# Kernel optimization log

Hardware: AMD Instinct MI355X
Metric: run time of the kernel (lower is better)

The kernel has to match this reference:

```python
import jax, jax.numpy as jnp
import numpy as np

H, NH, L, S, B, V = 512, 8, 6, 2048, 2, 32000
DH = H // NH
EPS = 1e-5


def posenc(h, s):
    pos = jnp.arange(s, dtype=jnp.float32)[:, None]
    div = jnp.power(10000.0, jnp.arange(0, h, 2, dtype=jnp.float32) / h)
    pe = jnp.zeros((s, h), dtype=jnp.float32)
    pe = pe.at[:, 0::2].set(jnp.sin(pos / div))
    pe = pe.at[:, 1::2].set(jnp.cos(pos / div))
    return pe


def layernorm(x, g, b):
    mu = jnp.mean(x, axis=-1, keepdims=True)
    var = jnp.mean(jnp.square(x - mu), axis=-1, keepdims=True)
    return (x - mu) * jax.lax.rsqrt(var + EPS) * g + b


def setup_inputs() -> dict:
    key = jax.random.key(0)
    ks = jax.random.split(key, 16)
    sc = 0.02
    return {
        "src": jax.random.randint(ks[0], (B, S), 0, V),
        "mask": jnp.ones((B, 1, 1, S), dtype=jnp.int32),
        "emb": jax.random.normal(ks[1], (V, H), jnp.float32) * sc,
        "Wq": jax.random.normal(ks[2], (L, H, H), jnp.float32) * sc,
        "bq": jnp.zeros((L, H), jnp.float32),
        "Wk": jax.random.normal(ks[3], (L, H, H), jnp.float32) * sc,
        "bk": jnp.zeros((L, H), jnp.float32),
        "Wv": jax.random.normal(ks[4], (L, H, H), jnp.float32) * sc,
        "bv": jnp.zeros((L, H), jnp.float32),
        "Wo": jax.random.normal(ks[5], (L, H, H), jnp.float32) * sc,
        "bo": jnp.zeros((L, H), jnp.float32),
        "gamma": jnp.ones((L, H), jnp.float32),
        "beta": jnp.zeros((L, H), jnp.float32),
        "W1": jax.random.normal(ks[6], (L, H, 4 * H), jnp.float32) * sc,
        "b1": jnp.zeros((L, 4 * H), jnp.float32),
        "W2": jax.random.normal(ks[7], (L, 4 * H, H), jnp.float32) * sc,
        "b2": jnp.zeros((L, H), jnp.float32),
    }


def reference(src, mask, emb, Wq, bq, Wk, bk, Wv, bv, Wo, bo, gamma, beta, W1, b1, W2, b2):
    x = emb[src] + posenc(H, S)[None, :, :]  # [B,S,H]
    for i in range(L):
        q = (x @ Wq[i] + bq[i]).reshape(B, S, NH, DH).transpose(0, 2, 1, 3)
        k = (x @ Wk[i] + bk[i]).reshape(B, S, NH, DH).transpose(0, 2, 1, 3)
        v = (x @ Wv[i] + bv[i]).reshape(B, S, NH, DH).transpose(0, 2, 1, 3)
        scores = jnp.einsum("bhqd,bhkd->bhqk", q, k) / jnp.sqrt(jnp.float32(DH))
        scores = jnp.where(mask == 0, jnp.float32(-1e20), scores)
        attn = jax.nn.softmax(scores, axis=-1)
        av = jnp.einsum("bhqk,bhkd->bhqd", attn, v)
        attn_out = av.transpose(0, 2, 1, 3).reshape(B, S, H) @ Wo[i] + bo[i]
        # NOTE: same LayerNorm params applied to both sublayers (as in source)
        res = x + layernorm(attn_out, gamma[i], beta[i])
        ffn = jax.nn.relu(res @ W1[i] + b1[i]) @ W2[i] + b2[i]
        x = res + layernorm(ffn, gamma[i], beta[i])
    return x
```

## Files before the change

### kernel.cpp

```cpp
#include <hip/hip_runtime.h>
#include <math.h>

#define HDIM 512
#define NHEAD 8
#define NLAYER 6
#define SEQ 2048
#define BATCH 2
#define DHEAD 64
#define TOKENS (BATCH*SEQ)
#define FFND (4*HDIM)
#define QSTR 1536

typedef unsigned short u16;
typedef __attribute__((ext_vector_type(8))) short short8;
typedef __attribute__((ext_vector_type(4))) float f32x4;

__device__ __forceinline__ u16 f2b(float f) {
  unsigned u = __float_as_uint(f);
  u += 0x7FFFu + ((u >> 16) & 1u);
  return (u16)(u >> 16);
}

__device__ __forceinline__ void gload_lds16(const u16* g, u16* l) {
  __builtin_amdgcn_global_load_lds((const __attribute__((address_space(1))) void*)g,
                                   (__attribute__((address_space(3))) void*)l, 16, 0, 0);
}

__global__ void embed_pe(const int* __restrict__ src, const float* __restrict__ emb,
                         float* __restrict__ X, u16* __restrict__ Xb) {
  int tok = blockIdx.x;
  int lane = threadIdx.x;
  int s = tok & (SEQ - 1);
  int c0 = lane * 8;
  const float* e = emb + (long)src[tok] * HDIM + c0;
  float v[8];
#pragma unroll
  for (int j = 0; j < 8; j++) {
    int c = c0 + j;
    float arg = (float)s * exp2f(-(float)(c & ~1) * 0.02595256917f);
    v[j] = e[j] + ((c & 1) ? cosf(arg) : sinf(arg));
  }
  float* xp = X + (long)tok * HDIM + c0;
#pragma unroll
  for (int j = 0; j < 8; j++) xp[j] = v[j];
  u16 hb[8];
#pragma unroll
  for (int j = 0; j < 8; j++) hb[j] = f2b(v[j]);
  uint4 pk;
  pk.x = hb[0] | ((unsigned)hb[1] << 16);
  pk.y = hb[2] | ((unsigned)hb[3] << 16);
  pk.z = hb[4] | ((unsigned)hb[5] << 16);
  pk.w = hb[6] | ((unsigned)hb[7] << 16);
  *(uint4*)(Xb + (long)tok * HDIM + c0) = pk;
}

__global__ __launch_bounds__(256) void prep_weights(
    const float* __restrict__ Wq, const float* __restrict__ Wk, const float* __restrict__ Wv,
    const float* __restrict__ Wo, const float* __restrict__ W1, const float* __restrict__ W2,
    const float* __restrict__ bq, const float* __restrict__ bk, const float* __restrict__ bv,
    u16* __restrict__ Wqkvt, u16* __restrict__ Wot, u16* __restrict__ W1t, u16* __restrict__ W2t,
    float* __restrict__ bqkv) {
  int t = blockIdx.x;
  int tid = threadIdx.x;
  if (t == 768) {
    for (int i = tid; i < 1536; i += 256)
      bqkv[i] = (i < 512) ? bq[i] : (i < 1024) ? bk[i - 512] : bv[i - 1024];
    return;
  }
  const float* src; u16* dst; int K, N, kt, nt; long drow0 = 0;
  if (t < 192)      { int m = t / 64, r = t % 64; src = (m==0)?Wq:(m==1)?Wk:Wv; dst = Wqkvt; drow0 = (long)m*512; K=512;  N=512;  kt=r/8;  nt=r%8; }
  else if (t < 256) { int r = t - 192; src = Wo; dst = Wot; K=512;  N=512;  kt=r/8;  nt=r%8; }
  else if (t < 512) { int r = t - 256; src = W1; dst = W1t; K=512;  N=2048; kt=r/32; nt=r%32; }
  else              { int r = t - 512; src = W2; dst = W2t; K=2048; N=512;  kt=r/8;  nt=r%8; }
  __shared__ __align__(16) u16 Lt[64 * 72];
  int kl = tid >> 2;
#pragma unroll
  for (int rr = 0; rr < 4; rr++) {
    int cl = (tid & 3) * 4 + rr * 16;
    float4 v = *(const float4*)(src + (long)(kt * 64 + kl) * N + nt * 64 + cl);
    Lt[(cl + 0) * 72 + kl] = f2b(v.x);
    Lt[(cl + 1) * 72 + kl] = f2b(v.y);
    Lt[(cl + 2) * 72 + kl] = f2b(v.z);
    Lt[(cl + 3) * 72 + kl] = f2b(v.w);
  }
  __syncthreads();
  int nl = tid >> 2;
  int kc = (tid & 3) * 16;
  u16* dp = dst + (drow0 + nt * 64 + nl) * (long)K + kt * 64 + kc;
  *(uint4*)dp       = *(const uint4*)&Lt[nl * 72 + kc];
  *(uint4*)(dp + 8) = *(const uint4*)&Lt[nl * 72 + kc + 8];
}

__global__ __launch_bounds__(256) void vtranspose(const u16* __restrict__ QKV,
                                                  u16* __restrict__ Vtb) {
  __shared__ __align__(16) u16 Lt[64 * 72];
  int tid = threadIdx.x;
  int bh = blockIdx.y, b = bh >> 3, h = bh & 7;
  int s0 = blockIdx.x * 64;
  const u16* vsrc = QKV + (long)(b * SEQ + s0) * QSTR + 1024 + h * DHEAD;
  int key = tid >> 2, dc = (tid & 3) * 16;
  const u16* vp = vsrc + (long)key * QSTR + dc;
  uint4 v0 = *(const uint4*)vp;
  uint4 v1 = *(const uint4*)(vp + 8);
  unsigned vr[8] = { v0.x, v0.y, v0.z, v0.w, v1.x, v1.y, v1.z, v1.w };
#pragma unroll
  for (int j = 0; j < 8; j++) {
    Lt[(dc + 2 * j) * 72 + key]     = (u16)vr[j];
    Lt[(dc + 2 * j + 1) * 72 + key] = (u16)(vr[j] >> 16);
  }
  __syncthreads();
  int d = tid >> 2, kc = (tid & 3) * 16;
  u16* dst = Vtb + ((long)bh * DHEAD + d) * SEQ + s0 + kc;
  *(uint4*)dst       = *(const uint4*)&Lt[d * 72 + kc];
  *(uint4*)(dst + 8) = *(const uint4*)&Lt[d * 72 + kc + 8];
}

template <int BN, int KSPLIT, bool RELU, bool WF32, bool WB16>
__global__ __launch_bounds__(256) void gemm_tn(const u16* __restrict__ A,
                                               const u16* __restrict__ Bt,
                                               const float* __restrict__ bias,
                                               float* __restrict__ Cf,
                                               u16* __restrict__ Cb,
                                               int M, int N, int K) {
  constexpr int NF = BN / 32;
  __shared__ __align__(16) u16 As[2][128 * 32];
  __shared__ __align__(16) u16 Bs[2][BN * 32];
  int tid = threadIdx.x;
  int wave = tid >> 6, lane = tid & 63;
  int ln = lane & 15, hi = lane >> 4;
  int wm = wave >> 1, wn = wave & 1;
  int m0 = blockIdx.y * 128, n0 = blockIdx.x * BN;
  int z = (KSPLIT > 1) ? blockIdx.z : 0;
  int Ks = K / KSPLIT;
  const u16* Ab = A + z * Ks;
  const u16* Bb = Bt + z * Ks;

  f32x4 acc[4][NF] = {};

  int srow = lane >> 2;
  int skc  = (lane & 3) * 8;

  auto issue = [&](int kt, int buf) {
    int k0 = kt * 32;
#pragma unroll
    for (int j = 0; j < 2; j++) {
      int row = (wave * 2 + j) * 16 + srow;
      gload_lds16(Ab + (long)(m0 + row) * K + k0 + skc, &As[buf][row * 32 + skc]);
    }
#pragma unroll
    for (int j = 0; j < BN / 64; j++) {
      int row = (wave * (BN / 64) + j) * 16 + srow;
      gload_lds16(Bb + (long)(n0 + row) * K + k0 + skc, &Bs[buf][row * 32 + skc]);
    }
  };

  int NT = Ks / 32;
  issue(0, 0);
  __syncthreads();
  for (int kt = 0; kt < NT; kt++) {
    int buf = kt & 1;
    if (kt + 1 < NT) issue(kt + 1, buf ^ 1);
    short8 af[4], bf[NF];
#pragma unroll
    for (int mt = 0; mt < 4; mt++)
      af[mt] = *(const short8*)&As[buf][(wm * 64 + mt * 16 + ln) * 32 + 8 * hi];
#pragma unroll
    for (int nt = 0; nt < NF; nt++)
      bf[nt] = *(const short8*)&Bs[buf][(wn * (BN / 2) + nt * 16 + ln) * 32 + 8 * hi];
#pragma unroll
    for (int mt = 0; mt < 4; mt++)
#pragma unroll
      for (int nt = 0; nt < NF; nt++)
        acc[mt][nt] = __builtin_amdgcn_mfma_f32_16x16x32_bf16(af[mt], bf[nt], acc[mt][nt], 0, 0, 0);
    __syncthreads();
  }

  float* Cz = WF32 ? (Cf + (long)z * M * N) : nullptr;
#pragma unroll
  for (int mt = 0; mt < 4; mt++)
#pragma unroll
    for (int nt = 0; nt < NF; nt++)
#pragma unroll
      for (int r = 0; r < 4; r++) {
        int row = m0 + wm * 64 + mt * 16 + hi * 4 + r;
        int col = n0 + wn * (BN / 2) + nt * 16 + ln;
        float v = acc[mt][nt][r];
        if (KSPLIT == 1 || z == 0) v += bias[col];
        if (RELU) v = fmaxf(v, 0.0f);
        if (WF32) Cz[(long)row * N + col] = v;
        if (WB16) Cb[(long)row * N + col] = f2b(v);
      }
}

__global__ __launch_bounds__(256) void attention(const u16* __restrict__ QKV,
                                                 const u16* __restrict__ Vtb,
                                                 const int* __restrict__ mask,
                                                 u16* __restrict__ Og) {
  __shared__ __align__(16) u16 Ks[2][2][64 * 32];
  __shared__ __align__(16) u16 Vs[2][2][64 * 32];
  __shared__ __align__(16) u16 P[4 * 16 * 72];
  int tid = threadIdx.x, w = tid >> 6, lane = tid & 63;
  int ln = lane & 15, hi = lane >> 4;
  int bh = blockIdx.y, b = bh >> 3, h = bh & 7;
  int q0 = blockIdx.x * 64 + w * 16;
  const u16* qbase = QKV + (long)b * SEQ * QSTR + h * DHEAD;
  const u16* kbase = qbase + 512;
  const u16* vtbase = Vtb + (long)bh * DHEAD * SEQ;
  const int* mrow = mask + b * SEQ;
  u16* Pw = P + w * 16 * 72;

  short8 qf[2];
#pragma unroll
  for (int ks = 0; ks < 2; ks++)
    qf[ks] = *(const short8*)(qbase + (long)(q0 + ln) * QSTR + ks * 32 + 8 * hi);

  f32x4 o[4] = {};
  float lst[4] = {0.0f, 0.0f, 0.0f, 0.0f};

  int srow = w * 16 + (lane >> 2);
  int sc = (lane & 3) * 8;

  auto issue = [&](int t, int buf) {
    long kk = (long)t * 64;
    const u16* kg = kbase + (kk + srow) * QSTR + sc;
    gload_lds16(kg,      &Ks[buf][0][srow * 32 + sc]);
    gload_lds16(kg + 32, &Ks[buf][1][srow * 32 + sc]);
    const u16* vg = vtbase + (long)srow * SEQ + kk + sc;
    gload_lds16(vg,      &Vs[buf][0][srow * 32 + sc]);
    gload_lds16(vg + 32, &Vs[buf][1][srow * 32 + sc]);
  };

  const int NT = SEQ / 64;
  issue(0, 0);
  __syncthreads();
  for (int t = 0; t < NT; t++) {
    int buf = t & 1;
    if (t + 1 < NT) issue(t + 1, buf ^ 1);
    int k0 = t * 64;

    f32x4 s[4] = {};
#pragma unroll
    for (int ks = 0; ks < 2; ks++)
#pragma unroll
      for (int nt = 0; nt < 4; nt++) {
        short8 bf = *(const short8*)&Ks[buf][ks][(nt * 16 + ln) * 32 + 8 * hi];
        s[nt] = __builtin_amdgcn_mfma_f32_16x16x32_bf16(qf[ks], bf, s[nt], 0, 0, 0);
      }
    int mv[4];
#pragma unroll
    for (int nt = 0; nt < 4; nt++) mv[nt] = mrow[k0 + nt * 16 + ln];
#pragma unroll
    for (int r = 0; r < 4; r++) {
#pragma unroll
      for (int nt = 0; nt < 4; nt++) {
        float p = (mv[nt] == 0) ? 0.0f : __expf(s[nt][r] * 0.125f);
        lst[r] += p;
        Pw[(hi * 4 + r) * 72 + ((nt * 16 + ln) ^ (8 * hi))] = f2b(p);
      }
    }
    short8 pa[2];
#pragma unroll
    for (int ka = 0; ka < 2; ka++)
      pa[ka] = *(const short8*)&Pw[ln * 72 + (ka * 32 + ((8 * hi) ^ (8 * (ln >> 2))))];
#pragma unroll
    for (int nt = 0; nt < 4; nt++) {
      short8 bv0 = *(const short8*)&Vs[buf][0][(nt * 16 + ln) * 32 + 8 * hi];
      short8 bv1 = *(const short8*)&Vs[buf][1][(nt * 16 + ln) * 32 + 8 * hi];
      o[nt] = __builtin_amdgcn_mfma_f32_16x16x32_bf16(pa[0], bv0, o[nt], 0, 0, 0);
      o[nt] = __builtin_amdgcn_mfma_f32_16x16x32_bf16(pa[1], bv1, o[nt], 0, 0, 0);
    }
    __syncthreads();
  }

#pragma unroll
  for (int r = 0; r < 4; r++) {
    float l = lst[r];
    l += __shfl_xor(l, 1);
    l += __shfl_xor(l, 2);
    l += __shfl_xor(l, 4);
    l += __shfl_xor(l, 8);
    lst[r] = 1.0f / l;
  }

  u16* obase = Og + (long)b * SEQ * HDIM + h * DHEAD;
#pragma unroll
  for (int r = 0; r < 4; r++) {
    int srow2 = q0 + hi * 4 + r;
#pragma unroll
    for (int nt = 0; nt < 4; nt++)
      obase[(long)srow2 * HDIM + nt * 16 + ln] = f2b(o[nt][r] * lst[r]);
  }
}

__global__ __launch_bounds__(256) void ln_residual(const float* __restrict__ Xin,
                                                   const float* __restrict__ T0,
                                                   const float* __restrict__ T1,
                                                   const float* __restrict__ gamma,
                                                   const float* __restrict__ beta,
                                                   float* __restrict__ Xout,
                                                   u16* __restrict__ Xb) {
  int tid = threadIdx.x, w = tid >> 6, lane = tid & 63;
  int row = blockIdx.x * 4 + w;
  const float* t0 = T0 + (long)row * HDIM;
  const float* t1 = T1 + (long)row * HDIM;
  int c0 = lane * 8;
  float v[8];
  {
    float4 a0 = *(const float4*)(t0 + c0);
    float4 b0 = *(const float4*)(t0 + c0 + 4);
    float4 a1 = *(const float4*)(t1 + c0);
    float4 b1 = *(const float4*)(t1 + c0 + 4);
    v[0] = a0.x + a1.x; v[1] = a0.y + a1.y; v[2] = a0.z + a1.z; v[3] = a0.w + a1.w;
    v[4] = b0.x + b1.x; v[5] = b0.y + b1.y; v[6] = b0.z + b1.z; v[7] = b0.w + b1.w;
  }
  float sum = 0.0f;
#pragma unroll
  for (int j = 0; j < 8; j++) sum += v[j];
#pragma unroll
  for (int off = 32; off; off >>= 1) sum += __shfl_xor(sum, off);
  float mu = sum * (1.0f / HDIM);
  float sq = 0.0f;
#pragma unroll
  for (int j = 0; j < 8; j++) { float d = v[j] - mu; sq += d * d; }
#pragma unroll
  for (int off = 32; off; off >>= 1) sq += __shfl_xor(sq, off);
  float rs = rsqrtf(sq * (1.0f / HDIM) + 1e-5f);
  const float* xin = Xin + (long)row * HDIM + c0;
  float* xout = Xout + (long)row * HDIM + c0;
  u16 hb[8];
#pragma unroll
  for (int j = 0; j < 8; j++) {
    int c = c0 + j;
    float y = xin[j] + (v[j] - mu) * rs * gamma[c] + beta[c];
    xout[j] = y;
    hb[j] = f2b(y);
  }
  uint4 pk;
  pk.x = hb[0] | ((unsigned)hb[1] << 16);
  pk.y = hb[2] | ((unsigned)hb[3] << 16);
  pk.z = hb[4] | ((unsigned)hb[5] << 16);
  pk.w = hb[6] | ((unsigned)hb[7] << 16);
  *(uint4*)(Xb + (long)row * HDIM + c0) = pk;
}

extern "C" void kernel_launch(void* const* d_in, const int* in_sizes, int n_in,
                              void* d_out, int out_size, void* d_ws, size_t ws_size,
                              hipStream_t stream) {
  const int*   src   = (const int*)d_in[0];
  const int*   mask  = (const int*)d_in[1];
  const float* emb   = (const float*)d_in[2];
  const float* Wq    = (const float*)d_in[3];
  const float* bq    = (const float*)d_in[4];
  const float* Wk    = (const float*)d_in[5];
  const float* bk    = (const float*)d_in[6];
  const float* Wv    = (const float*)d_in[7];
  const float* bv    = (const float*)d_in[8];
  const float* Wo    = (const float*)d_in[9];
  const float* bo    = (const float*)d_in[10];
  const float* gamma = (const float*)d_in[11];
  const float* beta  = (const float*)d_in[12];
  const float* W1    = (const float*)d_in[13];
  const float* b1    = (const float*)d_in[14];
  const float* W2    = (const float*)d_in[15];
  const float* b2    = (const float*)d_in[16];

  char* ws = (char*)d_ws;
  float* X     = (float*)(ws);
  u16*   Xb    = (u16*)(ws + (8ll << 20));
  u16*   QKVb  = (u16*)(ws + (12ll << 20));
  u16*   Mb    = (u16*)(ws + (12ll << 20));
  u16*   AVb   = (u16*)(ws + (24ll << 20));
  float* T     = (float*)(ws + (28ll << 20));
  u16*   Wqkvt = (u16*)(ws + (44ll << 20));
  u16*   Wot   = (u16*)(ws + (45ll << 20) + (512ll << 10));
  u16*   W1t   = (u16*)(ws + (46ll << 20));
  u16*   W2t   = (u16*)(ws + (48ll << 20));
  float* bqkv  = (float*)(ws + (50ll << 20));
  u16*   Vtb   = (u16*)(ws + (51ll << 20));
  float* T1    = T + (long)TOKENS * HDIM;

  embed_pe<<<dim3(TOKENS), dim3(64), 0, stream>>>(src, emb, X, Xb);

  for (int i = 0; i < NLAYER; i++) {
    long wo = (long)i * HDIM * HDIM;
    prep_weights<<<dim3(769), 256, 0, stream>>>(
        Wq + wo, Wk + wo, Wv + wo, Wo + wo,
        W1 + (long)i * HDIM * FFND, W2 + (long)i * FFND * HDIM,
        bq + i * HDIM, bk + i * HDIM, bv + i * HDIM,
        Wqkvt, Wot, W1t, W2t, bqkv);

    gemm_tn<128, 1, false, false, true><<<dim3(QSTR / 128, TOKENS / 128), 256, 0, stream>>>(
        Xb, Wqkvt, bqkv, nullptr, QKVb, TOKENS, QSTR, HDIM);

    vtranspose<<<dim3(SEQ / 64, BATCH * NHEAD), 256, 0, stream>>>(QKVb, Vtb);

    attention<<<dim3(SEQ / 64, BATCH * NHEAD), 256, 0, stream>>>(QKVb, Vtb, mask, AVb);

    gemm_tn<64, 2, false, true, false><<<dim3(HDIM / 64, TOKENS / 128, 2), 256, 0, stream>>>(
        AVb, Wot, bo + i * HDIM, T, nullptr, TOKENS, HDIM, HDIM);

    ln_residual<<<dim3(TOKENS / 4), 256, 0, stream>>>(X, T, T1, gamma + i * HDIM,
                                                      beta + i * HDIM, X, Xb);

    gemm_tn<128, 1, true, false, true><<<dim3(FFND / 128, TOKENS / 128), 256, 0, stream>>>(
        Xb, W1t, b1 + (long)i * FFND, nullptr, Mb, TOKENS, FFND, HDIM);

    gemm_tn<64, 2, false, true, false><<<dim3(HDIM / 64, TOKENS / 128, 2), 256, 0, stream>>>(
        Mb, W2t, b2 + i * HDIM, T, nullptr, TOKENS, HDIM, FFND);

    ln_residual<<<dim3(TOKENS / 4), 256, 0, stream>>>(X, T, T1, gamma + i * HDIM,
                                                      beta + i * HDIM, X, Xb);
  }

  hipMemcpyAsync(d_out, X, (size_t)TOKENS * HDIM * sizeof(float),
                 hipMemcpyDeviceToDevice, stream);
}
```

Before: 1.064 ms.

## Compute transposed S^T tiles in attention to keep P in registers, skipping LDS

The attention kernel now computes K·Q^T, so the score tile comes out transposed and each lane's probabilities can be packed straight into the B operand of the PV MFMA. A cross-lane shuffle replaces the round trip through shared memory for P. K/V tiles move to an XOR-swizzled 64-wide LDS layout with permuted key rows. Mask loads are vectorised and row sums are reduced once at the end. The output is staged through LDS for coalesced 16-byte stores, and bf16 packing uses the hardware v_cvt_pk_bf16_f32 instruction. The intent is to cut LDS traffic, bank conflicts and store inefficiency, at the cost of tricky lane/key index mapping that must be exactly right.

New measurement: 1.070 ms. About the same (+0.6%).

```diff
diff --git a/kernel.cpp b/kernel.cpp
--- a/kernel.cpp
+++ b/kernel.cpp
@@ -19,6 +19,12 @@
   unsigned u = __float_as_uint(f);
   u += 0x7FFFu + ((u >> 16) & 1u);
   return (u16)(u >> 16);
+}
+
+__device__ __forceinline__ unsigned cvtpk_bf16(float lo, float hi) {
+  unsigned r;
+  asm("v_cvt_pk_bf16_f32 %0, %1, %2" : "=v"(r) : "v"(lo), "v"(hi));
+  return r;
 }
 
 __device__ __forceinline__ void gload_lds16(const u16* g, u16* l) {
@@ -196,99 +202,130 @@
                                                  const u16* __restrict__ Vtb,
                                                  const int* __restrict__ mask,
                                                  u16* __restrict__ Og) {
-  __shared__ __align__(16) u16 Ks[2][2][64 * 32];
-  __shared__ __align__(16) u16 Vs[2][2][64 * 32];
-  __shared__ __align__(16) u16 P[4 * 16 * 72];
+  __shared__ __align__(16) u16 Ks[2][64 * 64];
+  __shared__ __align__(16) u16 Vs[2][64 * 64];
   int tid = threadIdx.x, w = tid >> 6, lane = tid & 63;
   int ln = lane & 15, hi = lane >> 4;
+  int h0 = hi & 1, h1 = hi >> 1, ln7 = ln & 7;
   int bh = blockIdx.y, b = bh >> 3, h = bh & 7;
   int q0 = blockIdx.x * 64 + w * 16;
   const u16* qbase = QKV + (long)b * SEQ * QSTR + h * DHEAD;
   const u16* kbase = qbase + 512;
   const u16* vtbase = Vtb + (long)bh * DHEAD * SEQ;
   const int* mrow = mask + b * SEQ;
-  u16* Pw = P + w * 16 * 72;
 
   short8 qf[2];
 #pragma unroll
   for (int ks = 0; ks < 2; ks++)
     qf[ks] = *(const short8*)(qbase + (long)(q0 + ln) * QSTR + ks * 32 + 8 * hi);
 
+  int sr0 = tid >> 3, sc = tid & 7;
+  const u16 *kp0, *kp1, *vp0, *vp1;
+  {
+    int r1 = sr0 + 32;
+    int key0 = (sr0 & 7) | ((sr0 & 0x18) << 1) | ((sr0 & 0x20) >> 2);
+    int key1 = (r1 & 7) | ((r1 & 0x18) << 1) | ((r1 & 0x20) >> 2);
+    kp0 = kbase + (long)key0 * QSTR + (sc ^ (sr0 & 7)) * 8;
+    kp1 = kbase + (long)key1 * QSTR + (sc ^ (r1 & 7)) * 8;
+    vp0 = vtbase + (long)sr0 * SEQ + (sc ^ (sr0 & 7)) * 8;
+    vp1 = vtbase + (long)r1 * SEQ + (sc ^ (r1 & 7)) * 8;
+  }
+  int d0 = sr0 * 64 + sc * 8, d1 = d0 + 2048;
+
+  auto issue = [&](int t, int buf) {
+    long ko = (long)t * (64 * QSTR);
+    int vo = t * 64;
+    gload_lds16(kp0 + ko, &Ks[buf][d0]);
+    gload_lds16(kp1 + ko, &Ks[buf][d1]);
+    gload_lds16(vp0 + vo, &Vs[buf][d0]);
+    gload_lds16(vp1 + vo, &Vs[buf][d1]);
+  };
+
   f32x4 o[4] = {};
-  float lst[4] = {0.0f, 0.0f, 0.0f, 0.0f};
-
-  int srow = w * 16 + (lane >> 2);
-  int sc = (lane & 3) * 8;
-
-  auto issue = [&](int t, int buf) {
-    long kk = (long)t * 64;
-    const u16* kg = kbase + (kk + srow) * QSTR + sc;
-    gload_lds16(kg,      &Ks[buf][0][srow * 32 + sc]);
-    gload_lds16(kg + 32, &Ks[buf][1][srow * 32 + sc]);
-    const u16* vg = vtbase + (long)srow * SEQ + kk + sc;
-    gload_lds16(vg,      &Vs[buf][0][srow * 32 + sc]);
-    gload_lds16(vg + 32, &Vs[buf][1][srow * 32 + sc]);
-  };
-
+  float lsum = 0.0f;
   const int NT = SEQ / 64;
   issue(0, 0);
   __syncthreads();
   for (int t = 0; t < NT; t++) {
     int buf = t & 1;
+    const int* mbase = mrow + t * 64 + 16 * h1 + 4 * h0;
+    int4 mv[4];
+    mv[0] = *(const int4*)(mbase);
+    mv[1] = *(const int4*)(mbase + 32);
+    mv[2] = *(const int4*)(mbase + 8);
+    mv[3] = *(const int4*)(mbase + 40);
     if (t + 1 < NT) issue(t + 1, buf ^ 1);
-    int k0 = t * 64;
 
     f32x4 s[4] = {};
 #pragma unroll
     for (int ks = 0; ks < 2; ks++)
 #pragma unroll
-      for (int nt = 0; nt < 4; nt++) {
-        short8 bf = *(const short8*)&Ks[buf][ks][(nt * 16 + ln) * 32 + 8 * hi];
-        s[nt] = __builtin_amdgcn_mfma_f32_16x16x32_bf16(qf[ks], bf, s[nt], 0, 0, 0);
+      for (int kb = 0; kb < 4; kb++) {
+        short8 kf = *(const short8*)&Ks[buf][(kb * 16 + ln) * 64 + (((ks << 2) + hi) ^ ln7) * 8];
+        s[kb] = __builtin_amdgcn_mfma_f32_16x16x32_bf16(kf, qf[ks], s[kb], 0, 0, 0);
       }
-    int mv[4];
-#pragma unroll
-    for (int nt = 0; nt < 4; nt++) mv[nt] = mrow[k0 + nt * 16 + ln];
-#pragma unroll
-    for (int r = 0; r < 4; r++) {
-#pragma unroll
-      for (int nt = 0; nt < 4; nt++) {
-        float p = (mv[nt] == 0) ? 0.0f : __expf(s[nt][r] * 0.125f);
-        lst[r] += p;
-        Pw[(hi * 4 + r) * 72 + ((nt * 16 + ln) ^ (8 * hi))] = f2b(p);
+
+    unsigned D[4][2];
+#pragma unroll
+    for (int kb = 0; kb < 4; kb++) {
+      float p[4];
+#pragma unroll
+      for (int r = 0; r < 4; r++) {
+        float pv = __expf(s[kb][r] * 0.125f);
+        int m = (&mv[kb].x)[r];
+        pv = m ? pv : 0.0f;
+        lsum += pv;
+        p[r] = pv;
       }
+      D[kb][0] = cvtpk_bf16(p[0], p[1]);
+      D[kb][1] = cvtpk_bf16(p[2], p[3]);
     }
-    short8 pa[2];
-#pragma unroll
-    for (int ka = 0; ka < 2; ka++)
-      pa[ka] = *(const short8*)&Pw[ln * 72 + (ka * 32 + ((8 * hi) ^ (8 * (ln >> 2))))];
-#pragma unroll
-    for (int nt = 0; nt < 4; nt++) {
-      short8 bv0 = *(const short8*)&Vs[buf][0][(nt * 16 + ln) * 32 + 8 * hi];
-      short8 bv1 = *(const short8*)&Vs[buf][1][(nt * 16 + ln) * 32 + 8 * hi];
-      o[nt] = __builtin_amdgcn_mfma_f32_16x16x32_bf16(pa[0], bv0, o[nt], 0, 0, 0);
-      o[nt] = __builtin_amdgcn_mfma_f32_16x16x32_bf16(pa[1], bv1, o[nt], 0, 0, 0);
+
+    short8 pb[2];
+#pragma unroll
+    for (int ks = 0; ks < 2; ks++) {
+      unsigned own0 = h0 ? D[2 + ks][0] : D[ks][0];
+      unsigned own1 = h0 ? D[2 + ks][1] : D[ks][1];
+      unsigned snd0 = h0 ? D[ks][0] : D[2 + ks][0];
+      unsigned snd1 = h0 ? D[ks][1] : D[2 + ks][1];
+      unsigned rc0 = (unsigned)__shfl_xor((int)snd0, 16);
+      unsigned rc1 = (unsigned)__shfl_xor((int)snd1, 16);
+      union { unsigned u[4]; short8 v; } pu;
+      pu.u[0] = h0 ? rc0 : own0;
+      pu.u[1] = h0 ? rc1 : own1;
+      pu.u[2] = h0 ? own0 : rc0;
+      pu.u[3] = h0 ? own1 : rc1;
+      pb[ks] = pu.v;
     }
+
+#pragma unroll
+    for (int ks = 0; ks < 2; ks++)
+#pragma unroll
+      for (int mb = 0; mb < 4; mb++) {
+        short8 vf = *(const short8*)&Vs[buf][(mb * 16 + ln) * 64 + (((ks << 2) + hi) ^ ln7) * 8];
+        o[mb] = __builtin_amdgcn_mfma_f32_16x16x32_bf16(vf, pb[ks], o[mb], 0, 0, 0);
+      }
     __syncthreads();
   }
 
-#pragma unroll
-  for (int r = 0; r < 4; r++) {
-    float l = lst[r];
-    l += __shfl_xor(l, 1);
-    l += __shfl_xor(l, 2);
-    l += __shfl_xor(l, 4);
-    l += __shfl_xor(l, 8);
-    lst[r] = 1.0f / l;
-  }
-
+  lsum += __shfl_xor(lsum, 16);
+  lsum += __shfl_xor(lsum, 32);
+  float rl = 1.0f / lsum;
+
+  u16* Ot = &Ks[0][0] + w * 1024;
+#pragma unroll
+  for (int mb = 0; mb < 4; mb++) {
+    *(unsigned*)&Ot[ln * 64 + mb * 16 + hi * 4 + 0] = cvtpk_bf16(o[mb][0] * rl, o[mb][1] * rl);
+    *(unsigned*)&Ot[ln * 64 + mb * 16 + hi * 4 + 2] = cvtpk_bf16(o[mb][2] * rl, o[mb][3] * rl);
+  }
+  __syncthreads();
   u16* obase = Og + (long)b * SEQ * HDIM + h * DHEAD;
 #pragma unroll
-  for (int r = 0; r < 4; r++) {
-    int srow2 = q0 + hi * 4 + r;
-#pragma unroll
-    for (int nt = 0; nt < 4; nt++)
-      obase[(long)srow2 * HDIM + nt * 16 + ln] = f2b(o[nt][r] * lst[r]);
+  for (int pass = 0; pass < 2; pass++) {
+    int row = (lane >> 3) + 8 * pass;
+    int c = lane & 7;
+    uint4 val = *(const uint4*)&Ot[row * 64 + c * 8];
+    *(uint4*)(obase + (long)(q0 + row) * HDIM + c * 8) = val;
   }
 }
 
```
